# Kernel optimization log

Hardware: AMD Instinct MI355X
Metric: run time of the kernel (lower is better)

Reference implementation:

```python
import jax, jax.numpy as jnp
import numpy as np

B, S, D_IN, D_OUT = 4, 2048, 4096, 4096
QMAX = 16  # 2**bits

def setup_inputs() -> dict:
    key = jax.random.key(0)
    k1, k2, k3, k4, k5 = jax.random.split(key, 5)
    x = jax.random.normal(k1, (B, S, D_IN), dtype=jnp.float32)
    weight_q = jax.random.randint(k2, (D_OUT, D_IN), 0, QMAX, dtype=jnp.int32)
    scale = jax.random.uniform(k3, (), dtype=jnp.float32) * 0.01 + 1e-4
    zero_point = jax.random.uniform(k4, (), dtype=jnp.float32) * QMAX
    bias = jax.random.normal(k5, (D_OUT,), dtype=jnp.float32)
    return {"x": x, "weight_q": weight_q, "scale": scale,
            "zero_point": zero_point, "bias": bias}

def reference(x, weight_q, scale, zero_point, bias):
    # Dequantize: w = (q - zero_point) * scale, then y = x @ w.T + b
    w = (weight_q.astype(jnp.float32) - zero_point) * scale  # [out, in]
    return jnp.einsum('bsi,oi->bso', x, w) + bias
```

## Files before the change

kernel.cpp:

```cpp
#include <hip/hip_runtime.h>
#include <cstdint>

#define M_DIM 8192
#define N_DIM 4096
#define K_DIM 4096
#define NT    32

typedef int i32x4 __attribute__((ext_vector_type(4)));

__device__ __forceinline__ void gload_lds16(const void* g, void* l) {
  __builtin_amdgcn_global_load_lds(
      (const __attribute__((address_space(1))) unsigned int*)(uintptr_t)g,
      (__attribute__((address_space(3))) unsigned int*)(uintptr_t)l,
      16, 0, 0);
}

__global__ __launch_bounds__(256) void prep_kernel(
    const float* __restrict__ x, const int* __restrict__ q,
    signed char* __restrict__ xq, signed char* __restrict__ wq8,
    float* __restrict__ sx, float* __restrict__ si) {
  const int tid  = threadIdx.x;
  const int lane = tid & 63;
  const int wv   = tid >> 6;
  if (blockIdx.x < 2048) {
    const int row = blockIdx.x * 4 + wv;
    const float* xr = x + (size_t)row * K_DIM;
    signed char* xo = xq + (size_t)row * K_DIM;
    float4 v[16];
    float amax = 0.f;
#pragma unroll
    for (int j = 0; j < 16; ++j) {
      v[j] = *(const float4*)(xr + j * 256 + lane * 4);
      amax = fmaxf(amax, fmaxf(fmaxf(fabsf(v[j].x), fabsf(v[j].y)),
                               fmaxf(fabsf(v[j].z), fabsf(v[j].w))));
    }
#pragma unroll
    for (int off = 32; off > 0; off >>= 1)
      amax = fmaxf(amax, __shfl_xor(amax, off, 64));
    const float inv = amax > 0.f ? 127.f / amax : 0.f;
    int isum = 0;
#pragma unroll
    for (int j = 0; j < 16; ++j) {
      int ix = __float2int_rn(v[j].x * inv);
      int iy = __float2int_rn(v[j].y * inv);
      int iz = __float2int_rn(v[j].z * inv);
      int iw = __float2int_rn(v[j].w * inv);
      isum += ix + iy + iz + iw;
      char4 o; o.x = (char)ix; o.y = (char)iy; o.z = (char)iz; o.w = (char)iw;
      *(char4*)(xo + j * 256 + lane * 4) = o;
    }
#pragma unroll
    for (int off = 32; off > 0; off >>= 1)
      isum += __shfl_xor(isum, off, 64);
    if (lane == 0) {
      sx[row] = amax * (1.f / 127.f);
      si[row] = (float)isum;
    }
  } else {
    const int bid = blockIdx.x - 2048;
    const size_t total  = (size_t)N_DIM * K_DIM;
    const size_t stride = (size_t)1024 * 4096;
    for (size_t base = (size_t)bid * 4096; base < total; base += stride) {
#pragma unroll
      for (int u = 0; u < 4; ++u) {
        const size_t idx = base + (size_t)u * 1024 + tid * 4;
        int4 w = *(const int4*)(q + idx);
        char4 o; o.x = (char)w.x; o.y = (char)w.y; o.z = (char)w.z; o.w = (char)w.w;
        *(char4*)(wq8 + idx) = o;
      }
    }
  }
}

__global__ __launch_bounds__(512) void qlinear_gemm_kernel(
    const signed char* __restrict__ A,
    const signed char* __restrict__ Bm,
    const float* __restrict__ sx,
    const float* __restrict__ si,
    const float* __restrict__ scale_p, const float* __restrict__ zp_p,
    const float* __restrict__ bias,
    float* __restrict__ out) {
  __shared__ signed char sA[2][2][16384];
  __shared__ signed char sB[2][2][16384];

  const int tid  = threadIdx.x;
  const int lane = tid & 63;
  const int w    = tid >> 6;
  const int wr   = w >> 2;
  const int wc   = w & 3;
  const int lr   = lane & 15;
  const int quad = lane >> 4;

  const int bid = blockIdx.x;
  const int swz = (bid & 7) * 64 + (bid >> 3);
  const int bm  = (swz >> 4) * 256;
  const int bn  = (swz & 15) * 256;

  const int srow = lane >> 3;
  const int cg   = (lane & 7) ^ srow;
  const signed char* aG = A  + (size_t)(bm + w * 8 + srow) * K_DIM + cg * 16;
  const signed char* bG = Bm + (size_t)(bn + w * 8 + srow) * K_DIM + cg * 16;
  const int dwoff = w * 1024;

#define STG_A(dst, h, c, t) \
  gload_lds16(aG + (size_t)((h) * 128 + (c) * 64) * K_DIM + (size_t)(t) * 128, \
              (dst) + (h) * 16384 + (c) * 8192 + dwoff)
#define STG_B(dst, h, c, t) \
  gload_lds16(bG + (size_t)((h) * 128 + (c) * 64) * K_DIM + (size_t)(t) * 128, \
              (dst) + (h) * 16384 + (c) * 8192 + dwoff)

  int off[2];
#pragma unroll
  for (int ks = 0; ks < 2; ++ks)
    off[ks] = lr * 128 + (((ks * 4 + quad) ^ (lr & 7)) * 16);

  i32x4 acc[8][4] = {};
  i32x4 afr[4][2];
  i32x4 bfr[4][2];

  {
    signed char* dA = &sA[0][0][0];
    signed char* dB = &sB[0][0][0];
    STG_B(dB, 0, 0, 0); STG_B(dB, 0, 1, 0);
    STG_B(dB, 1, 0, 0); STG_B(dB, 1, 1, 0);
    STG_A(dA, 0, 0, 0); STG_A(dA, 1, 0, 0);
    STG_A(dA, 0, 1, 0); STG_A(dA, 1, 1, 0);
  }

  for (int t = 0; t < NT; ++t) {
    const int buf = t & 1;
    const signed char* pA = &sA[buf][wr][0];
    const signed char* pB = &sB[buf][wc >> 1][0] + (wc & 1) * 8192;
    signed char* nA = &sA[buf ^ 1][0][0];
    signed char* nB = &sB[buf ^ 1][0][0];
    const bool st = (t + 1) < NT;
    const int tn = t + 1;

    asm volatile("s_waitcnt vmcnt(2)" ::: "memory");
    __builtin_amdgcn_s_barrier();
    if (st) { STG_B(nB, 0, 0, tn); STG_B(nB, 0, 1, tn);
              STG_B(nB, 1, 0, tn); STG_B(nB, 1, 1, tn); }
#pragma unroll
    for (int m = 0; m < 4; ++m)
      afr[m][0] = *(const i32x4*)(pA + m * 2048 + off[0]);
#pragma unroll
    for (int n = 0; n < 4; ++n)
      bfr[n][0] = *(const i32x4*)(pB + n * 2048 + off[0]);
    __builtin_amdgcn_sched_barrier(0);
#pragma unroll
    for (int m = 0; m < 4; ++m)
      afr[m][1] = *(const i32x4*)(pA + m * 2048 + off[1]);
#pragma unroll
    for (int n = 0; n < 4; ++n)
      bfr[n][1] = *(const i32x4*)(pB + n * 2048 + off[1]);
    __builtin_amdgcn_sched_barrier(0);
    asm volatile("s_waitcnt lgkmcnt(8)" ::: "memory");
    __builtin_amdgcn_sched_barrier(0);
    __builtin_amdgcn_s_setprio(1);
#pragma unroll
    for (int m = 0; m < 4; ++m)
#pragma unroll
      for (int n = 0; n < 4; ++n)
        acc[m][n] = __builtin_amdgcn_mfma_i32_16x16x64_i8(
            afr[m][0], bfr[n][0], acc[m][n], 0, 0, 0);
    __builtin_amdgcn_s_setprio(0);
    asm volatile("s_waitcnt lgkmcnt(0)" ::: "memory");
    __builtin_amdgcn_sched_barrier(0);
    __builtin_amdgcn_s_setprio(1);
#pragma unroll
    for (int m = 0; m < 4; ++m)
#pragma unroll
      for (int n = 0; n < 4; ++n)
        acc[m][n] = __builtin_amdgcn_mfma_i32_16x16x64_i8(
            afr[m][1], bfr[n][1], acc[m][n], 0, 0, 0);
    __builtin_amdgcn_s_setprio(0);

    if (st) asm volatile("s_waitcnt vmcnt(4)" ::: "memory");
    else    asm volatile("s_waitcnt vmcnt(0)" ::: "memory");
    __builtin_amdgcn_s_barrier();
    if (st) { STG_A(nA, 0, 0, tn); STG_A(nA, 1, 0, tn);
              STG_A(nA, 0, 1, tn); STG_A(nA, 1, 1, tn); }
#pragma unroll
    for (int m = 0; m < 4; ++m)
      afr[m][0] = *(const i32x4*)(pA + 8192 + m * 2048 + off[0]);
    __builtin_amdgcn_sched_barrier(0);
#pragma unroll
    for (int m = 0; m < 4; ++m)
      afr[m][1] = *(const i32x4*)(pA + 8192 + m * 2048 + off[1]);
    __builtin_amdgcn_sched_barrier(0);
    asm volatile("s_waitcnt lgkmcnt(4)" ::: "memory");
    __builtin_amdgcn_sched_barrier(0);
    __builtin_amdgcn_s_setprio(1);
#pragma unroll
    for (int m = 0; m < 4; ++m)
#pragma unroll
      for (int n = 0; n < 4; ++n)
        acc[4 + m][n] = __builtin_amdgcn_mfma_i32_16x16x64_i8(
            afr[m][0], bfr[n][0], acc[4 + m][n], 0, 0, 0);
    __builtin_amdgcn_s_setprio(0);
    asm volatile("s_waitcnt lgkmcnt(0)" ::: "memory");
    __builtin_amdgcn_sched_barrier(0);
    __builtin_amdgcn_s_setprio(1);
#pragma unroll
    for (int m = 0; m < 4; ++m)
#pragma unroll
      for (int n = 0; n < 4; ++n)
        acc[4 + m][n] = __builtin_amdgcn_mfma_i32_16x16x64_i8(
            afr[m][1], bfr[n][1], acc[4 + m][n], 0, 0, 0);
    __builtin_amdgcn_s_setprio(0);
  }
#undef STG_A
#undef STG_B

  const float scale = *scale_p;
  const float zp    = *zp_p;
#pragma unroll
  for (int i = 0; i < 8; ++i) {
    const int gm0 = bm + wr * 128 + i * 16 + quad * 4;
    float am[4], cm[4];
#pragma unroll
    for (int r = 0; r < 4; ++r) {
      am[r] = scale * sx[gm0 + r];
      cm[r] = -am[r] * zp * si[gm0 + r];
    }
#pragma unroll
    for (int j = 0; j < 4; ++j) {
      const int gn = bn + wc * 64 + j * 16 + lr;
      const float bb = bias[gn];
#pragma unroll
      for (int r = 0; r < 4; ++r)
        out[(size_t)(gm0 + r) * N_DIM + gn] =
            am[r] * (float)acc[i][j][r] + cm[r] + bb;
    }
  }
}

extern "C" void kernel_launch(void* const* d_in, const int* in_sizes, int n_in,
                              void* d_out, int out_size, void* d_ws, size_t ws_size,
                              hipStream_t stream) {
  const float* x     = (const float*)d_in[0];
  const int*   wq    = (const int*)d_in[1];
  const float* scale = (const float*)d_in[2];
  const float* zp    = (const float*)d_in[3];
  const float* bias  = (const float*)d_in[4];
  float* out = (float*)d_out;

  signed char* xq  = (signed char*)d_ws;
  signed char* wq8 = xq + (size_t)M_DIM * K_DIM;
  float* sx = (float*)(wq8 + (size_t)N_DIM * K_DIM);
  float* si = sx + M_DIM;

  prep_kernel<<<3072, 256, 0, stream>>>(x, wq, xq, wq8, sx, si);
  qlinear_gemm_kernel<<<512, 512, 0, stream>>>(xq, wq8, sx, si, scale, zp, bias, out);
}
```

Measured before the change: 385.5 us.

## Simplify GEMM main loop to single-barrier prefetch with occupancy hint

The main loop now issues the global-to-LDS prefetch of both A and B for the next K tile at the top of each iteration. It replaces the two split barriers, the partial vmcnt/lgkmcnt waits, the sched_barriers and the setprio hints with one vmcnt(0)-plus-barrier at the end of the iteration. The launch bounds now request two blocks per CU, which caps the register budget. The intent is to reduce synchronization and give the compiler freedom to schedule. The risks are register spills from the 128-register accumulator set and losing the hand-tuned interleaving of LDS reads with MFMA. The 128 KB of LDS per block probably prevents a second resident block anyway.

```diff
diff --git a/kernel.cpp b/kernel.cpp
--- a/kernel.cpp
+++ b/kernel.cpp
@@ -72,7 +72,7 @@
   }
 }
 
-__global__ __launch_bounds__(512) void qlinear_gemm_kernel(
+__global__ __launch_bounds__(512, 2) void qlinear_gemm_kernel(
     const signed char* __restrict__ A,
     const signed char* __restrict__ Bm,
     const float* __restrict__ sx,
@@ -115,8 +115,6 @@
     off[ks] = lr * 128 + (((ks * 4 + quad) ^ (lr & 7)) * 16);
 
   i32x4 acc[8][4] = {};
-  i32x4 afr[4][2];
-  i32x4 bfr[4][2];
 
   {
     signed char* dA = &sA[0][0][0];
@@ -126,6 +124,8 @@
     STG_A(dA, 0, 0, 0); STG_A(dA, 1, 0, 0);
     STG_A(dA, 0, 1, 0); STG_A(dA, 1, 1, 0);
   }
+  asm volatile("s_waitcnt vmcnt(0)" ::: "memory");
+  __builtin_amdgcn_s_barrier();
 
   for (int t = 0; t < NT; ++t) {
     const int buf = t & 1;
@@ -136,78 +136,55 @@
     const bool st = (t + 1) < NT;
     const int tn = t + 1;
 
-    asm volatile("s_waitcnt vmcnt(2)" ::: "memory");
-    __builtin_amdgcn_s_barrier();
-    if (st) { STG_B(nB, 0, 0, tn); STG_B(nB, 0, 1, tn);
-              STG_B(nB, 1, 0, tn); STG_B(nB, 1, 1, tn); }
-#pragma unroll
-    for (int m = 0; m < 4; ++m)
-      afr[m][0] = *(const i32x4*)(pA + m * 2048 + off[0]);
+    if (st) {
+      STG_B(nB, 0, 0, tn); STG_B(nB, 0, 1, tn);
+      STG_B(nB, 1, 0, tn); STG_B(nB, 1, 1, tn);
+      STG_A(nA, 0, 0, tn); STG_A(nA, 1, 0, tn);
+      STG_A(nA, 0, 1, tn); STG_A(nA, 1, 1, tn);
+    }
+    __builtin_amdgcn_sched_barrier(0);
+
+    i32x4 bfr[4][2], afr[4][2];
 #pragma unroll
     for (int n = 0; n < 4; ++n)
-      bfr[n][0] = *(const i32x4*)(pB + n * 2048 + off[0]);
-    __builtin_amdgcn_sched_barrier(0);
-#pragma unroll
-    for (int m = 0; m < 4; ++m)
-      afr[m][1] = *(const i32x4*)(pA + m * 2048 + off[1]);
-#pragma unroll
-    for (int n = 0; n < 4; ++n)
-      bfr[n][1] = *(const i32x4*)(pB + n * 2048 + off[1]);
-    __builtin_amdgcn_sched_barrier(0);
-    asm volatile("s_waitcnt lgkmcnt(8)" ::: "memory");
-    __builtin_amdgcn_sched_barrier(0);
-    __builtin_amdgcn_s_setprio(1);
+#pragma unroll
+      for (int ks = 0; ks < 2; ++ks)
+        bfr[n][ks] = *(const i32x4*)(pB + n * 2048 + off[ks]);
+#pragma unroll
+    for (int m = 0; m < 4; ++m)
+#pragma unroll
+      for (int ks = 0; ks < 2; ++ks)
+        afr[m][ks] = *(const i32x4*)(pA + m * 2048 + off[ks]);
+
 #pragma unroll
     for (int m = 0; m < 4; ++m)
 #pragma unroll
       for (int n = 0; n < 4; ++n)
-        acc[m][n] = __builtin_amdgcn_mfma_i32_16x16x64_i8(
-            afr[m][0], bfr[n][0], acc[m][n], 0, 0, 0);
-    __builtin_amdgcn_s_setprio(0);
-    asm volatile("s_waitcnt lgkmcnt(0)" ::: "memory");
-    __builtin_amdgcn_sched_barrier(0);
-    __builtin_amdgcn_s_setprio(1);
+#pragma unroll
+        for (int ks = 0; ks < 2; ++ks)
+          acc[m][n] = __builtin_amdgcn_mfma_i32_16x16x64_i8(
+              afr[m][ks], bfr[n][ks], acc[m][n], 0, 0, 0);
+
+    i32x4 afr2[4][2];
+#pragma unroll
+    for (int m = 0; m < 4; ++m)
+#pragma unroll
+      for (int ks = 0; ks < 2; ++ks)
+        afr2[m][ks] = *(const i32x4*)(pA + 8192 + m * 2048 + off[ks]);
+
 #pragma unroll
     for (int m = 0; m < 4; ++m)
 #pragma unroll
       for (int n = 0; n < 4; ++n)
-        acc[m][n] = __builtin_amdgcn_mfma_i32_16x16x64_i8(
-            afr[m][1], bfr[n][1], acc[m][n], 0, 0, 0);
-    __builtin_amdgcn_s_setprio(0);
-
-    if (st) asm volatile("s_waitcnt vmcnt(4)" ::: "memory");
-    else    asm volatile("s_waitcnt vmcnt(0)" ::: "memory");
-    __builtin_amdgcn_s_barrier();
-    if (st) { STG_A(nA, 0, 0, tn); STG_A(nA, 1, 0, tn);
-              STG_A(nA, 0, 1, tn); STG_A(nA, 1, 1, tn); }
-#pragma unroll
-    for (int m = 0; m < 4; ++m)
-      afr[m][0] = *(const i32x4*)(pA + 8192 + m * 2048 + off[0]);
-    __builtin_amdgcn_sched_barrier(0);
-#pragma unroll
-    for (int m = 0; m < 4; ++m)
-      afr[m][1] = *(const i32x4*)(pA + 8192 + m * 2048 + off[1]);
-    __builtin_amdgcn_sched_barrier(0);
-    asm volatile("s_waitcnt lgkmcnt(4)" ::: "memory");
-    __builtin_amdgcn_sched_barrier(0);
-    __builtin_amdgcn_s_setprio(1);
-#pragma unroll
-    for (int m = 0; m < 4; ++m)
-#pragma unroll
-      for (int n = 0; n < 4; ++n)
-        acc[4 + m][n] = __builtin_amdgcn_mfma_i32_16x16x64_i8(
-            afr[m][0], bfr[n][0], acc[4 + m][n], 0, 0, 0);
-    __builtin_amdgcn_s_setprio(0);
-    asm volatile("s_waitcnt lgkmcnt(0)" ::: "memory");
-    __builtin_amdgcn_sched_barrier(0);
-    __builtin_amdgcn_s_setprio(1);
-#pragma unroll
-    for (int m = 0; m < 4; ++m)
-#pragma unroll
-      for (int n = 0; n < 4; ++n)
-        acc[4 + m][n] = __builtin_amdgcn_mfma_i32_16x16x64_i8(
-            afr[m][1], bfr[n][1], acc[4 + m][n], 0, 0, 0);
-    __builtin_amdgcn_s_setprio(0);
+#pragma unroll
+        for (int ks = 0; ks < 2; ++ks)
+          acc[4 + m][n] = __builtin_amdgcn_mfma_i32_16x16x64_i8(
+              afr2[m][ks], bfr[n][ks], acc[4 + m][n], 0, 0, 0);
+
+    if (st) {
+      asm volatile("s_waitcnt vmcnt(0)" ::: "memory");
+      __builtin_amdgcn_s_barrier();
+    }
   }
 #undef STG_A
 #undef STG_B
```

New measurement: 391.7 us. About the same (+1.6%).
